# Optimization experiments

Hardware: AMD Instinct MI355X
Metric: run time of the kernel (lower is better)

The kernel has to match this reference:

```python
import jax, jax.numpy as jnp
import numpy as np

B, S, D, H = 4, 2048, 1024, 16
DK = D // H


def setup_inputs() -> dict:
    key = jax.random.key(0)
    ks = jax.random.split(key, 11)
    scale = 1.0 / np.sqrt(D)
    inp = {
        "query": jax.random.normal(ks[0], (B, S, D), dtype=jnp.float32),
        "key": jax.random.normal(ks[1], (B, S, D), dtype=jnp.float32),
        "value": jax.random.normal(ks[2], (B, S, D), dtype=jnp.float32),
        "Wq": jax.random.normal(ks[3], (D, D), dtype=jnp.float32) * scale,
        "bq": jnp.zeros((D,), dtype=jnp.float32),
        "Wk": jax.random.normal(ks[4], (D, D), dtype=jnp.float32) * scale,
        "bk": jnp.zeros((D,), dtype=jnp.float32),
        "Wv": jax.random.normal(ks[5], (D, D), dtype=jnp.float32) * scale,
        "bv": jnp.zeros((D,), dtype=jnp.float32),
        "Wo": jax.random.normal(ks[6], (D, D), dtype=jnp.float32) * scale,
        "bo": jnp.zeros((D,), dtype=jnp.float32),
    }
    return inp


def reference(query, key, value, Wq, bq, Wk, bk, Wv, bv, Wo, bo):
    # QKV projections -> [B, H, S, DK]
    def proj(x, W, b):
        return (x @ W + b).reshape(B, -1, H, DK).transpose(0, 2, 1, 3)

    q = proj(query, Wq, bq)
    k = proj(key, Wk, bk)
    v = proj(value, Wv, bv)

    # scores: [B, H, S, S] (explicitly materialized, as in the source)
    scores = jnp.einsum("bhqd,bhkd->bhqk", q, k) / jnp.sqrt(jnp.float32(DK))
    p_attn = jax.nn.softmax(scores, axis=-1)  # dropout = identity (eval)
    x = jnp.einsum("bhqk,bhkd->bhqd", p_attn, v)

    # merge heads -> output projection
    x = x.transpose(0, 2, 1, 3).reshape(B, -1, H * DK)
    return x @ Wo + bo
```

## Files before the change

### kernel.cpp

```cpp
#include <hip/hip_runtime.h>


#define B_ 4
#define S_ 2048
#define D_ 1024
#define H_ 16
#define M_ 8192

typedef unsigned short u16;
typedef unsigned int u32;
typedef float f32x4 __attribute__((ext_vector_type(4)));
typedef float f32x16 __attribute__((ext_vector_type(16)));
typedef __bf16 bf16x8 __attribute__((ext_vector_type(8)));
typedef u32 u32x4 __attribute__((ext_vector_type(4)));

__device__ __forceinline__ u16 f2bf(float f) {
  unsigned int x = __float_as_uint(f);
  x = (x + 0x7fffu + ((x >> 16) & 1u)) >> 16;
  return (u16)x;
}

__device__ __forceinline__ f32x4 mfma16(bf16x8 a, bf16x8 b, f32x4 c) {
  return __builtin_amdgcn_mfma_f32_16x16x32_bf16(a, b, c, 0, 0, 0);
}
__device__ __forceinline__ f32x16 mfma32(bf16x8 a, bf16x8 b, f32x16 c) {
  return __builtin_amdgcn_mfma_f32_32x32x16_bf16(a, b, c, 0, 0, 0);
}
__device__ __forceinline__ u32 cvtpk_bf16(float lo, float hi) {
  u32 r;
  asm("v_cvt_pk_bf16_f32 %0, %1, %2" : "=v"(r) : "v"(lo), "v"(hi));
  return r;
}
__device__ __forceinline__ void gload_lds16(const u16* g, u16* l) {
  __builtin_amdgcn_global_load_lds((const __attribute__((address_space(1))) void*)g,
                                   (__attribute__((address_space(3))) void*)l, 16, 0, 0);
}

__global__ __launch_bounds__(256) void cast_bf16_kernel(const float4* __restrict__ in,
                                                        ushort4* __restrict__ out, int n4) {
  int i = blockIdx.x * 256 + threadIdx.x;
  int stride = gridDim.x * 256;
  for (; i < n4; i += stride) {
    float4 v = in[i];
    ushort4 o;
    o.x = f2bf(v.x); o.y = f2bf(v.y); o.z = f2bf(v.z); o.w = f2bf(v.w);
    out[i] = o;
  }
}

__global__ __launch_bounds__(256) void wtrans_kernel(const float* __restrict__ W,
                                                     u16* __restrict__ WT) {
  __shared__ float tile[32][33];
  int k0 = blockIdx.x * 32, n0 = blockIdx.y * 32;
  int t = threadIdx.x, c = t & 31, r0 = t >> 5;
#pragma unroll
  for (int i = 0; i < 4; ++i)
    tile[r0 + i * 8][c] = W[(size_t)(k0 + r0 + i * 8) * D_ + n0 + c];
  __syncthreads();
#pragma unroll
  for (int i = 0; i < 4; ++i)
    WT[(size_t)(n0 + r0 + i * 8) * D_ + k0 + c] = f2bf(tile[c][r0 + i * 8]);
}

__global__ __launch_bounds__(256) void vtrans_kernel(const u16* __restrict__ Vp,
                                                     u16* __restrict__ Vt) {
  __shared__ u16 tile[64][65];
  int bx = blockIdx.x;
  int bh = bx >> 5;
  int s0 = (bx & 31) * 64;
  int b = bh >> 4, h = bh & 15;
  int t = threadIdx.x, c = t & 63, r0 = t >> 6;
#pragma unroll
  for (int i = 0; i < 16; ++i) {
    int s = r0 + i * 4;
    tile[s][c] = Vp[(size_t)(b * S_ + s0 + s) * D_ + h * 64 + c];
  }
  __syncthreads();
#pragma unroll
  for (int i = 0; i < 16; ++i) {
    int dk = r0 + i * 4;
    Vt[((size_t)bh * 64 + dk) * S_ + s0 + c] = tile[c][dk];
  }
}

template <bool OUT_F32>
__global__ __launch_bounds__(256) void gemm_kernel(const u16* __restrict__ A,
                                                   const u16* __restrict__ BT,
                                                   const float* __restrict__ bias,
                                                   void* __restrict__ out) {
  __shared__ __align__(16) u16 ldsA[128 * 64];
  __shared__ __align__(16) u16 ldsB[128 * 64];
  int bx = blockIdx.x;
  int swz = (bx & 7) * 64 + (bx >> 3);
  int bm = swz >> 3, bn = swz & 7;
  int t = threadIdx.x, w = t >> 6, lane = t & 63;
  int wm = w >> 1, wn = w & 1;
  int l15 = lane & 15, hi = lane >> 4;

  f32x4 acc[4][4];
#pragma unroll
  for (int m = 0; m < 4; ++m)
#pragma unroll
    for (int n = 0; n < 4; ++n) acc[m][n] = (f32x4){0.f, 0.f, 0.f, 0.f};

  int srow = w * 32 + (lane >> 3);
  int schunk = lane & 7;
  const u16* Ag = A + (size_t)(bm * 128 + srow) * D_ + schunk * 8;
  const u16* Bg = BT + (size_t)(bn * 128 + srow) * D_ + schunk * 8;
  u16* lA = ldsA + w * 32 * 64;
  u16* lB = ldsB + w * 32 * 64;

  for (int kk = 0; kk < D_; kk += 64) {
    __syncthreads();
#pragma unroll
    for (int i = 0; i < 4; ++i) {
      gload_lds16(Ag + kk + i * 8 * D_, lA + i * 8 * 64);
      gload_lds16(Bg + kk + i * 8 * D_, lB + i * 8 * 64);
    }
    __syncthreads();
#pragma unroll
    for (int ks = 0; ks < 2; ++ks) {
      bf16x8 af[4], bfr[4];
#pragma unroll
      for (int m = 0; m < 4; ++m)
        af[m] = *(const bf16x8*)(ldsA + (wm * 64 + m * 16 + l15) * 64 + (ks * 4 + hi) * 8);
#pragma unroll
      for (int n = 0; n < 4; ++n)
        bfr[n] = *(const bf16x8*)(ldsB + (wn * 64 + n * 16 + l15) * 64 + (ks * 4 + hi) * 8);
#pragma unroll
      for (int m = 0; m < 4; ++m)
#pragma unroll
        for (int n = 0; n < 4; ++n)
          acc[m][n] = mfma16(af[m], bfr[n], acc[m][n]);
    }
  }

#pragma unroll
  for (int m = 0; m < 4; ++m)
#pragma unroll
    for (int n = 0; n < 4; ++n) {
      int row = bm * 128 + wm * 64 + m * 16 + hi * 4;
      int col = bn * 128 + wn * 64 + n * 16 + l15;
      float bv = bias[col];
#pragma unroll
      for (int r = 0; r < 4; ++r) {
        float v = acc[m][n][r] + bv;
        if (OUT_F32)
          ((float*)out)[(size_t)(row + r) * D_ + col] = v;
        else
          ((u16*)out)[(size_t)(row + r) * D_ + col] = f2bf(v);
      }
    }
}

__global__ __launch_bounds__(512) void attn_kernel(const u16* __restrict__ Qp,
                                                   const u16* __restrict__ Kp,
                                                   const u16* __restrict__ Vt,
                                                   u16* __restrict__ ctx) {
  __shared__ __align__(16) u16 Kl[128 * 64];
  __shared__ __align__(16) u16 Vl[64 * 128];

  int bx = blockIdx.x;
  int bh = (bx & 7) * 8 + (bx >> 6);
  int qt = (bx >> 3) & 7;
  int b = bh >> 4, h = bh & 15;

  int t = threadIdx.x, w = t >> 6, lane = t & 63;
  int l31 = lane & 31, hh = lane >> 5;
  int qglob = qt * 256 + w * 32;

  bf16x8 qf[4];
  {
    const u16* qptr = Qp + (size_t)(b * S_ + qglob + l31) * D_ + h * 64;
#pragma unroll
    for (int ks = 0; ks < 4; ++ks) {
      bf16x8 v = *(const bf16x8*)(qptr + ks * 16 + hh * 8);
#pragma unroll
      for (int j = 0; j < 8; ++j) v[j] = (__bf16)((float)v[j] * 0.125f);
      qf[ks] = v;
    }
  }

  float m = -1e30f, l = 0.f;
  f32x16 O0, O1;
#pragma unroll
  for (int i = 0; i < 16; ++i) { O0[i] = 0.f; O1[i] = 0.f; }

  const u16* Kbase = Kp + (size_t)(b * S_) * D_ + h * 64;
  const u16* Vbase = Vt + (size_t)bh * 64 * S_;
  int krow = t >> 3, kc = t & 7;
  int vrow = t >> 4, vc = t & 15;
  u32x4 kreg0, kreg1, vreg0, vreg1;
  kreg0 = *(const u32x4*)(Kbase + (size_t)(krow)*D_ + kc * 8);
  kreg1 = *(const u32x4*)(Kbase + (size_t)(krow + 64) * D_ + kc * 8);
  vreg0 = *(const u32x4*)(Vbase + (size_t)(vrow)*S_ + vc * 8);
  vreg1 = *(const u32x4*)(Vbase + (size_t)(vrow + 32) * S_ + vc * 8);

  for (int kt = 0; kt < 16; ++kt) {
    __syncthreads();
    *(u32x4*)(Kl + krow * 64 + ((kc ^ (krow & 7)) << 3)) = kreg0;
    *(u32x4*)(Kl + (krow + 64) * 64 + ((kc ^ (krow & 7)) << 3)) = kreg1;
    *(u32x4*)(Vl + vrow * 128 + (((vc & 8) | ((vc ^ vrow) & 7)) << 3)) = vreg0;
    *(u32x4*)(Vl + (vrow + 32) * 128 + (((vc & 8) | ((vc ^ vrow) & 7)) << 3)) = vreg1;
    if (kt < 15) {
      kreg0 = *(const u32x4*)(Kbase + (size_t)(kt * 128 + 128 + krow) * D_ + kc * 8);
      kreg1 = *(const u32x4*)(Kbase + (size_t)(kt * 128 + 192 + krow) * D_ + kc * 8);
      vreg0 = *(const u32x4*)(Vbase + (size_t)(vrow)*S_ + kt * 128 + 128 + vc * 8);
      vreg1 = *(const u32x4*)(Vbase + (size_t)(vrow + 32) * S_ + kt * 128 + 128 + vc * 8);
    }
    __syncthreads();

    f32x16 pct[4];
#pragma unroll
    for (int ct = 0; ct < 4; ++ct) {
      f32x16 p;
#pragma unroll
      for (int i = 0; i < 16; ++i) p[i] = 0.f;
#pragma unroll
      for (int ks = 0; ks < 4; ++ks) {
        int key = ct * 32 + l31;
        int cl = 2 * ks + hh;
        bf16x8 kf = *(const bf16x8*)(Kl + key * 64 + ((cl ^ (key & 7)) << 3));
        p = mfma32(kf, qf[ks], p);
      }
      pct[ct] = p;
    }

    float pm = pct[0][0];
#pragma unroll
    for (int ct = 0; ct < 4; ++ct)
#pragma unroll
      for (int i = 0; i < 16; ++i) pm = fmaxf(pm, pct[ct][i]);
    pm = fmaxf(pm, __shfl_xor(pm, 32, 64));

    if (!__all(pm <= m)) {
      float mn = fmaxf(m, pm);
      float alpha = __expf(m - mn);
      m = mn;
      l *= alpha;
#pragma unroll
      for (int i = 0; i < 16; ++i) {
        float a = __shfl(alpha, (i & 3) + 8 * (i >> 2) + 4 * hh, 64);
        O0[i] *= a;
        O1[i] *= a;
      }
    }

    float ls = 0.f;
#pragma unroll
    for (int ct = 0; ct < 4; ++ct)
#pragma unroll
      for (int i = 0; i < 16; ++i) {
        float e = __expf(pct[ct][i] - m);
        pct[ct][i] = e;
        ls += e;
      }
    l += ls + __shfl_xor(ls, 32, 64);

#pragma unroll
    for (int ct = 0; ct < 4; ++ct) {
#pragma unroll
      for (int ks2 = 0; ks2 < 2; ++ks2) {
        u32 A0 = cvtpk_bf16(pct[ct][8 * ks2 + 0], pct[ct][8 * ks2 + 1]);
        u32 A1 = cvtpk_bf16(pct[ct][8 * ks2 + 2], pct[ct][8 * ks2 + 3]);
        u32 B0 = cvtpk_bf16(pct[ct][8 * ks2 + 4], pct[ct][8 * ks2 + 5]);
        u32 B1 = cvtpk_bf16(pct[ct][8 * ks2 + 6], pct[ct][8 * ks2 + 7]);
        u32 s0 = __shfl_xor((int)(hh ? A0 : B0), 32, 64);
        u32 s1 = __shfl_xor((int)(hh ? A1 : B1), 32, 64);
        u32x4 fw;
        fw[0] = hh ? s0 : A0;
        fw[1] = hh ? s1 : A1;
        fw[2] = hh ? B0 : s0;
        fw[3] = hh ? B1 : s1;
        bf16x8 pf = __builtin_bit_cast(bf16x8, fw);
        int cl = ct * 4 + 2 * ks2 + hh;
#pragma unroll
        for (int dkh = 0; dkh < 2; ++dkh) {
          int dk = l31 + dkh * 32;
          bf16x8 vf = *(const bf16x8*)(Vl + dk * 128 + (((cl & 8) | ((cl ^ dk) & 7)) << 3));
          if (dkh == 0) O0 = mfma32(pf, vf, O0);
          else          O1 = mfma32(pf, vf, O1);
        }
      }
    }
  }

#pragma unroll
  for (int r = 0; r < 16; ++r) {
    int ql = (r & 3) + 8 * (r >> 2) + 4 * hh;
    float lr = __shfl(l, ql, 64);
    float inv = 1.0f / lr;
    u16* cp = ctx + (size_t)(b * S_ + qglob + ql) * D_ + h * 64;
    cp[l31] = f2bf(O0[r] * inv);
    cp[l31 + 32] = f2bf(O1[r] * inv);
  }
}

extern "C" void kernel_launch(void* const* d_in, const int* in_sizes, int n_in,
                              void* d_out, int out_size, void* d_ws, size_t ws_size,
                              hipStream_t stream) {
  const float* query = (const float*)d_in[0];
  const float* key   = (const float*)d_in[1];
  const float* value = (const float*)d_in[2];
  const float* Wq = (const float*)d_in[3];
  const float* bq = (const float*)d_in[4];
  const float* Wk = (const float*)d_in[5];
  const float* bk = (const float*)d_in[6];
  const float* Wv = (const float*)d_in[7];
  const float* bv = (const float*)d_in[8];
  const float* Wo = (const float*)d_in[9];
  const float* bo = (const float*)d_in[10];

  char* ws = (char*)d_ws;
  const size_t WT_BYTES  = (size_t)D_ * D_ * 2;
  const size_t MAT_BYTES = (size_t)M_ * D_ * 2;
  u16* WTq = (u16*)(ws);
  u16* WTk = (u16*)(ws + WT_BYTES);
  u16* WTv = (u16*)(ws + 2 * WT_BYTES);
  u16* WTo = (u16*)(ws + 3 * WT_BYTES);
  u16* Xb  = (u16*)(ws + 4 * WT_BYTES);
  u16* Qp  = (u16*)(ws + 4 * WT_BYTES + MAT_BYTES);
  u16* Kp  = (u16*)(ws + 4 * WT_BYTES + 2 * MAT_BYTES);
  u16* Vp  = (u16*)(ws + 4 * WT_BYTES + 3 * MAT_BYTES);
  u16* Vt  = Xb;
  u16* ctx = Vp;

  dim3 blk(256);
  dim3 wgrid(32, 32);
  wtrans_kernel<<<wgrid, blk, 0, stream>>>(Wq, WTq);
  wtrans_kernel<<<wgrid, blk, 0, stream>>>(Wk, WTk);
  wtrans_kernel<<<wgrid, blk, 0, stream>>>(Wv, WTv);
  wtrans_kernel<<<wgrid, blk, 0, stream>>>(Wo, WTo);

  const int n4 = M_ * D_ / 4;
  cast_bf16_kernel<<<2048, blk, 0, stream>>>((const float4*)query, (ushort4*)Xb, n4);
  gemm_kernel<false><<<512, blk, 0, stream>>>(Xb, WTq, bq, Qp);
  cast_bf16_kernel<<<2048, blk, 0, stream>>>((const float4*)key, (ushort4*)Xb, n4);
  gemm_kernel<false><<<512, blk, 0, stream>>>(Xb, WTk, bk, Kp);
  cast_bf16_kernel<<<2048, blk, 0, stream>>>((const float4*)value, (ushort4*)Xb, n4);
  gemm_kernel<false><<<512, blk, 0, stream>>>(Xb, WTv, bv, Vp);
  vtrans_kernel<<<2048, blk, 0, stream>>>(Vp, Vt);
  attn_kernel<<<512, dim3(512), 0, stream>>>(Qp, Kp, Vt, ctx);
  gemm_kernel<true><<<512, blk, 0, stream>>>(ctx, WTo, bo, d_out);
}
```

Before: 403.5 us.

## Fuse fp32-to-bf16 cast into QKV GEMM, batch launches, use exp2 softmax

```diff
diff --git a/kernel.cpp b/kernel.cpp
--- a/kernel.cpp
+++ b/kernel.cpp
@@ -12,6 +12,7 @@
 typedef float f32x4 __attribute__((ext_vector_type(4)));
 typedef float f32x16 __attribute__((ext_vector_type(16)));
 typedef __bf16 bf16x8 __attribute__((ext_vector_type(8)));
+typedef u32 u32x2 __attribute__((ext_vector_type(2)));
 typedef u32 u32x4 __attribute__((ext_vector_type(4)));
 
 __device__ __forceinline__ u16 f2bf(float f) {
@@ -36,21 +37,15 @@
                                    (__attribute__((address_space(3))) void*)l, 16, 0, 0);
 }
 
-__global__ __launch_bounds__(256) void cast_bf16_kernel(const float4* __restrict__ in,
-                                                        ushort4* __restrict__ out, int n4) {
-  int i = blockIdx.x * 256 + threadIdx.x;
-  int stride = gridDim.x * 256;
-  for (; i < n4; i += stride) {
-    float4 v = in[i];
-    ushort4 o;
-    o.x = f2bf(v.x); o.y = f2bf(v.y); o.z = f2bf(v.z); o.w = f2bf(v.w);
-    out[i] = o;
-  }
-}
-
-__global__ __launch_bounds__(256) void wtrans_kernel(const float* __restrict__ W,
-                                                     u16* __restrict__ WT) {
+__global__ __launch_bounds__(256) void wtrans_kernel(
+    const float* __restrict__ W0, const float* __restrict__ W1,
+    const float* __restrict__ W2, const float* __restrict__ W3,
+    u16* __restrict__ T0, u16* __restrict__ T1,
+    u16* __restrict__ T2, u16* __restrict__ T3) {
   __shared__ float tile[32][33];
+  int z = blockIdx.z;
+  const float* W = z == 0 ? W0 : z == 1 ? W1 : z == 2 ? W2 : W3;
+  u16* WT = z == 0 ? T0 : z == 1 ? T1 : z == 2 ? T2 : T3;
   int k0 = blockIdx.x * 32, n0 = blockIdx.y * 32;
   int t = threadIdx.x, c = t & 31, r0 = t >> 5;
 #pragma unroll
@@ -83,11 +78,88 @@
   }
 }
 
-template <bool OUT_F32>
-__global__ __launch_bounds__(256) void gemm_kernel(const u16* __restrict__ A,
-                                                   const u16* __restrict__ BT,
-                                                   const float* __restrict__ bias,
-                                                   void* __restrict__ out) {
+__global__ __launch_bounds__(256) void gemm_qkv_kernel(
+    const float* __restrict__ Aq, const float* __restrict__ Ak, const float* __restrict__ Av,
+    const u16* __restrict__ BTq, const u16* __restrict__ BTk, const u16* __restrict__ BTv,
+    const float* __restrict__ bq, const float* __restrict__ bk, const float* __restrict__ bv,
+    u16* __restrict__ oq, u16* __restrict__ ok, u16* __restrict__ ov) {
+  __shared__ __align__(16) u16 ldsA[128 * 64];
+  __shared__ __align__(16) u16 ldsB[128 * 64];
+  int y = blockIdx.y;
+  const float* A  = y == 0 ? Aq : y == 1 ? Ak : Av;
+  const u16* BT   = y == 0 ? BTq : y == 1 ? BTk : BTv;
+  const float* bias = y == 0 ? bq : y == 1 ? bk : bv;
+  u16* out        = y == 0 ? oq : y == 1 ? ok : ov;
+
+  int bx = blockIdx.x;
+  int swz = (bx & 7) * 64 + (bx >> 3);
+  int bm = swz >> 3, bn = swz & 7;
+  int t = threadIdx.x, w = t >> 6, lane = t & 63;
+  int wm = w >> 1, wn = w & 1;
+  int l15 = lane & 15, hi = lane >> 4;
+
+  f32x4 acc[4][4];
+#pragma unroll
+  for (int m = 0; m < 4; ++m)
+#pragma unroll
+    for (int n = 0; n < 4; ++n) acc[m][n] = (f32x4){0.f, 0.f, 0.f, 0.f};
+
+  int srow = w * 32 + (lane >> 3);
+  int schunk = lane & 7;
+  const u16* Bg = BT + (size_t)(bn * 128 + srow) * D_ + schunk * 8;
+  u16* lB = ldsB + w * 32 * 64;
+
+  int arow = t >> 4, ac = t & 15;
+  const float* Ag = A + (size_t)(bm * 128 + arow) * D_ + ac * 4;
+
+  for (int kk = 0; kk < D_; kk += 64) {
+    __syncthreads();
+#pragma unroll
+    for (int i = 0; i < 4; ++i)
+      gload_lds16(Bg + kk + i * 8 * D_, lB + i * 8 * 64);
+#pragma unroll
+    for (int p = 0; p < 8; ++p) {
+      float4 v = *(const float4*)(Ag + kk + (size_t)p * 16 * D_);
+      u32x2 pk;
+      pk[0] = cvtpk_bf16(v.x, v.y);
+      pk[1] = cvtpk_bf16(v.z, v.w);
+      *(u32x2*)(ldsA + (arow + p * 16) * 64 + ac * 4) = pk;
+    }
+    __syncthreads();
+#pragma unroll
+    for (int ks = 0; ks < 2; ++ks) {
+      bf16x8 af[4], bfr[4];
+#pragma unroll
+      for (int m = 0; m < 4; ++m)
+        af[m] = *(const bf16x8*)(ldsA + (wm * 64 + m * 16 + l15) * 64 + (ks * 4 + hi) * 8);
+#pragma unroll
+      for (int n = 0; n < 4; ++n)
+        bfr[n] = *(const bf16x8*)(ldsB + (wn * 64 + n * 16 + l15) * 64 + (ks * 4 + hi) * 8);
+#pragma unroll
+      for (int m = 0; m < 4; ++m)
+#pragma unroll
+        for (int n = 0; n < 4; ++n)
+          acc[m][n] = mfma16(af[m], bfr[n], acc[m][n]);
+    }
+  }
+
+#pragma unroll
+  for (int m = 0; m < 4; ++m)
+#pragma unroll
+    for (int n = 0; n < 4; ++n) {
+      int row = bm * 128 + wm * 64 + m * 16 + hi * 4;
+      int col = bn * 128 + wn * 64 + n * 16 + l15;
+      float bv2 = bias[col];
+#pragma unroll
+      for (int r = 0; r < 4; ++r)
+        out[(size_t)(row + r) * D_ + col] = f2bf(acc[m][n][r] + bv2);
+    }
+}
+
+__global__ __launch_bounds__(256) void gemm_o_kernel(const u16* __restrict__ A,
+                                                     const u16* __restrict__ BT,
+                                                     const float* __restrict__ bias,
+                                                     float* __restrict__ out) {
   __shared__ __align__(16) u16 ldsA[128 * 64];
   __shared__ __align__(16) u16 ldsB[128 * 64];
   int bx = blockIdx.x;
@@ -143,13 +215,8 @@
       int col = bn * 128 + wn * 64 + n * 16 + l15;
       float bv = bias[col];
 #pragma unroll
-      for (int r = 0; r < 4; ++r) {
-        float v = acc[m][n][r] + bv;
-        if (OUT_F32)
-          ((float*)out)[(size_t)(row + r) * D_ + col] = v;
-        else
-          ((u16*)out)[(size_t)(row + r) * D_ + col] = f2bf(v);
-      }
+      for (int r = 0; r < 4; ++r)
+        out[(size_t)(row + r) * D_ + col] = acc[m][n][r] + bv;
     }
 }
 
@@ -176,7 +243,7 @@
     for (int ks = 0; ks < 4; ++ks) {
       bf16x8 v = *(const bf16x8*)(qptr + ks * 16 + hh * 8);
 #pragma unroll
-      for (int j = 0; j < 8; ++j) v[j] = (__bf16)((float)v[j] * 0.125f);
+      for (int j = 0; j < 8; ++j) v[j] = (__bf16)((float)v[j] * 0.18033688f);
       qf[ks] = v;
     }
   }
@@ -226,16 +293,18 @@
       pct[ct] = p;
     }
 
-    float pm = pct[0][0];
-#pragma unroll
-    for (int ct = 0; ct < 4; ++ct)
-#pragma unroll
-      for (int i = 0; i < 16; ++i) pm = fmaxf(pm, pct[ct][i]);
+    float pm0 = -1e30f, pm1 = -1e30f, pm2 = -1e30f, pm3 = -1e30f;
+#pragma unroll
+    for (int i = 0; i < 16; ++i) {
+      pm0 = fmaxf(pm0, pct[0][i]); pm1 = fmaxf(pm1, pct[1][i]);
+      pm2 = fmaxf(pm2, pct[2][i]); pm3 = fmaxf(pm3, pct[3][i]);
+    }
+    float pm = fmaxf(fmaxf(pm0, pm1), fmaxf(pm2, pm3));
     pm = fmaxf(pm, __shfl_xor(pm, 32, 64));
 
-    if (!__all(pm <= m)) {
+    if (!__all(pm - m <= 8.0f)) {
       float mn = fmaxf(m, pm);
-      float alpha = __expf(m - mn);
+      float alpha = exp2f(m - mn);
       m = mn;
       l *= alpha;
 #pragma unroll
@@ -246,15 +315,15 @@
       }
     }
 
-    float ls = 0.f;
-#pragma unroll
-    for (int ct = 0; ct < 4; ++ct)
-#pragma unroll
-      for (int i = 0; i < 16; ++i) {
-        float e = __expf(pct[ct][i] - m);
-        pct[ct][i] = e;
-        ls += e;
-      }
+    float ls0 = 0.f, ls1 = 0.f, ls2 = 0.f, ls3 = 0.f;
+#pragma unroll
+    for (int i = 0; i < 16; ++i) {
+      float e0 = exp2f(pct[0][i] - m); pct[0][i] = e0; ls0 += e0;
+      float e1 = exp2f(pct[1][i] - m); pct[1][i] = e1; ls1 += e1;
+      float e2 = exp2f(pct[2][i] - m); pct[2][i] = e2; ls2 += e2;
+      float e3 = exp2f(pct[3][i] - m); pct[3][i] = e3; ls3 += e3;
+    }
+    float ls = (ls0 + ls1) + (ls2 + ls3);
     l += ls + __shfl_xor(ls, 32, 64);
 
 #pragma unroll
@@ -318,28 +387,17 @@
   u16* WTk = (u16*)(ws + WT_BYTES);
   u16* WTv = (u16*)(ws + 2 * WT_BYTES);
   u16* WTo = (u16*)(ws + 3 * WT_BYTES);
-  u16* Xb  = (u16*)(ws + 4 * WT_BYTES);
+  u16* Vt  = (u16*)(ws + 4 * WT_BYTES);
   u16* Qp  = (u16*)(ws + 4 * WT_BYTES + MAT_BYTES);
   u16* Kp  = (u16*)(ws + 4 * WT_BYTES + 2 * MAT_BYTES);
   u16* Vp  = (u16*)(ws + 4 * WT_BYTES + 3 * MAT_BYTES);
-  u16* Vt  = Xb;
   u16* ctx = Vp;
 
   dim3 blk(256);
-  dim3 wgrid(32, 32);
-  wtrans_kernel<<<wgrid, blk, 0, stream>>>(Wq, WTq);
-  wtrans_kernel<<<wgrid, blk, 0, stream>>>(Wk, WTk);
-  wtrans_kernel<<<wgrid, blk, 0, stream>>>(Wv, WTv);
-  wtrans_kernel<<<wgrid, blk, 0, stream>>>(Wo, WTo);
-
-  const int n4 = M_ * D_ / 4;
-  cast_bf16_kernel<<<2048, blk, 0, stream>>>((const float4*)query, (ushort4*)Xb, n4);
-  gemm_kernel<false><<<512, blk, 0, stream>>>(Xb, WTq, bq, Qp);
-  cast_bf16_kernel<<<2048, blk, 0, stream>>>((const float4*)key, (ushort4*)Xb, n4);
-  gemm_kernel<false><<<512, blk, 0, stream>>>(Xb, WTk, bk, Kp);
-  cast_bf16_kernel<<<2048, blk, 0, stream>>>((const float4*)value, (ushort4*)Xb, n4);
-  gemm_kernel<false><<<512, blk, 0, stream>>>(Xb, WTv, bv, Vp);
+  wtrans_kernel<<<dim3(32, 32, 4), blk, 0, stream>>>(Wq, Wk, Wv, Wo, WTq, WTk, WTv, WTo);
+  gemm_qkv_kernel<<<dim3(512, 3), blk, 0, stream>>>(query, key, value, WTq, WTk, WTv,
+                                                    bq, bk, bv, Qp, Kp, Vp);
   vtrans_kernel<<<2048, blk, 0, stream>>>(Vp, Vt);
   attn_kernel<<<512, dim3(512), 0, stream>>>(Qp, Kp, Vt, ctx);
-  gemm_kernel<true><<<512, blk, 0, stream>>>(ctx, WTo, bo, d_out);
-}
+  gemm_o_kernel<<<512, blk, 0, stream>>>(ctx, WTo, bo, (float*)d_out);
+}
```

After: 429.8 us. 1.07x slower.
